# Performance work log

Hardware: AMD Instinct MI355X
Metric: run time of the kernel (lower is better)

Reference implementation:

```python
import jax, jax.numpy as jnp
import numpy as np

N, E, G, H, L, GD = 100000, 1600000, 64, 128, 3, 32
NEG_SLOPE = 0.2
EPS = 1e-5


def setup_inputs() -> dict:
    key = jax.random.key(0)
    ks = jax.random.split(key, 10)
    s = 1.0 / np.sqrt(H)
    return {
        "x": jax.random.normal(ks[0], (N, H), jnp.float32),
        "global_feat": jax.random.normal(ks[1], (G, GD), jnp.float32),
        "W_src": jax.random.normal(ks[2], (L, H, H), jnp.float32) * s,
        "W_dst": jax.random.normal(ks[3], (L, H, H), jnp.float32) * s,
        "att": jax.random.normal(ks[4], (L, H), jnp.float32) * s,
        "b_conv": jnp.zeros((L, H), jnp.float32),
        "gn_w": jnp.ones((L, H), jnp.float32),
        "gn_b": jnp.zeros((L, H), jnp.float32),
        "gn_ms": jnp.ones((L, H), jnp.float32),
        "W1": jax.random.normal(ks[5], (H * L + GD, H), jnp.float32) * (1.0 / np.sqrt(H * L + GD)),
        "b1": jnp.zeros((H,), jnp.float32),
        "W2": jax.random.normal(ks[6], (H, 1), jnp.float32) * s,
        "b2": jnp.zeros((1,), jnp.float32),
        "edge_index": jax.random.randint(ks[7], (2, E), 0, N, jnp.int64),
        "batch": jnp.sort(jax.random.randint(ks[8], (N,), 0, G, jnp.int64)),
    }


def reference(x, global_feat, W_src, W_dst, att, b_conv, gn_w, gn_b, gn_ms,
              W1, b1, W2, b2, edge_index, batch):
    n = x.shape[0]
    g = global_feat.shape[0]
    layers = W_src.shape[0]
    loops = jnp.arange(n, dtype=edge_index.dtype)
    src = jnp.concatenate([edge_index[0], loops])  # add_self_loops=True
    dst = jnp.concatenate([edge_index[1], loops])
    counts = jnp.maximum(
        jax.ops.segment_sum(jnp.ones((n,), x.dtype), batch, num_segments=g), 1.0)

    outs = []
    for l in range(layers):
        # --- GATv2Conv (heads=1) ---
        xl = x @ W_src[l]          # source transform [N,H]
        xr = x @ W_dst[l]          # target transform [N,H]
        e = jax.nn.leaky_relu(xl[src] + xr[dst], NEG_SLOPE) @ att[l]  # [Etot]
        emax = jax.ops.segment_max(e, dst, num_segments=n)
        ex = jnp.exp(e - emax[dst])
        denom = jax.ops.segment_sum(ex, dst, num_segments=n)
        alpha = ex / denom[dst]
        h = jax.ops.segment_sum(alpha[:, None] * xl[src], dst, num_segments=n) + b_conv[l]
        # --- GraphNorm ---
        mean = jax.ops.segment_sum(h, batch, num_segments=g) / counts[:, None]
        sub = h - gn_ms[l] * mean[batch]
        var = jax.ops.segment_sum(sub * sub, batch, num_segments=g) / counts[:, None]
        h = gn_w[l] * sub * jax.lax.rsqrt(var[batch] + EPS) + gn_b[l]
        x = jax.nn.relu(h)
        # --- global_mean_pool ---
        outs.append(jax.ops.segment_sum(x, batch, num_segments=g) / counts[:, None])

    hcat = jnp.concatenate(outs + [global_feat], axis=1)  # JK cat + global feats
    z = jax.nn.relu(hcat @ W1 + b1)  # dropout = identity (eval)
    return z @ W2 + b2
```

## Files before the change

### kernel.cpp

```cpp
#include <hip/hip_runtime.h>
#include <hip/hip_bf16.h>
#include <math.h>

#define N_    100000
#define E_    1600000
#define ETOT_ 1700000
#define G_    64
#define H_    128
#define GH_   8192
#define L_    3
#define GD_   32
#define NEG_  0.2f
#define EPS_  1e-5f

#define NBUK_ 391
#define CH_   2048
#define MCH_  782

typedef unsigned short ushort_t;
typedef unsigned int uint_t;
typedef __attribute__((ext_vector_type(4))) float f32x4;
typedef __attribute__((ext_vector_type(8))) short bf16x8;
typedef __attribute__((ext_vector_type(8))) unsigned short ushort8;

__device__ __forceinline__ ushort_t bfb(float f) {
    __hip_bfloat16 h = __float2bfloat16(f);
    return *reinterpret_cast<ushort_t*>(&h);
}
__device__ __forceinline__ float uf(ushort_t u) {
    return __uint_as_float(((uint_t)u) << 16);
}


__global__ void k_init(float* pooled, float* gsum, float* gsq, int* gstart,
                       const int* __restrict__ batch) {
    int i = blockIdx.x * 256 + threadIdx.x;
    if (i < L_ * GH_) { pooled[i] = 0.f; gsum[i] = 0.f; gsq[i] = 0.f; }
    if (i <= G_) {
        int lo = 0, hi = N_;
        while (lo < hi) { int mid = (lo + hi) >> 1; if (batch[mid] < i) lo = mid + 1; else hi = mid; }
        gstart[i] = lo;
    }
}


__global__ __launch_bounds__(256) void k_bcount(const int* __restrict__ edst, int* __restrict__ C) {
    __shared__ int hist[NBUK_];
    int t = threadIdx.x, m = blockIdx.x;
    for (int i = t; i < NBUK_; i += 256) hist[i] = 0;
    __syncthreads();
    int base = m * CH_;
#pragma unroll
    for (int j = 0; j < CH_ / 256; j++) {
        int e = base + j * 256 + t;
        if (e < E_) atomicAdd(&hist[edst[e] >> 8], 1);
    }
    __syncthreads();
    for (int i = t; i < NBUK_; i += 256) C[i * MCH_ + m] = hist[i];
}

__global__ __launch_bounds__(1024) void k_bscan(int* __restrict__ C, int* __restrict__ bucketEdges) {
    __shared__ int arr[1024];
    int b = blockIdx.x, t = threadIdx.x;
    int v = (t < MCH_) ? C[b * MCH_ + t] : 0;
    arr[t] = v;
    __syncthreads();
    for (int off = 1; off < 1024; off <<= 1) {
        int x = (t >= off) ? arr[t - off] : 0;
        __syncthreads();
        arr[t] += x;
        __syncthreads();
    }
    if (t < MCH_) C[b * MCH_ + t] = arr[t] - v;
    if (t == 1023) bucketEdges[b] = arr[1023];
}

__global__ __launch_bounds__(512) void k_bscan2(const int* __restrict__ bucketEdges,
                                                int* __restrict__ bstartE, int* __restrict__ bstartT,
                                                int* __restrict__ rowptr) {
    __shared__ int aE[512], aT[512];
    int t = threadIdx.x;
    int e = 0, tot = 0;
    if (t < NBUK_) {
        e = bucketEdges[t];
        int nib = N_ - t * 256; if (nib > 256) nib = 256;
        tot = e + nib;
    }
    aE[t] = e; aT[t] = tot;
    __syncthreads();
    for (int off = 1; off < 512; off <<= 1) {
        int xe = (t >= off) ? aE[t - off] : 0;
        int xt = (t >= off) ? aT[t - off] : 0;
        __syncthreads();
        aE[t] += xe; aT[t] += xt;
        __syncthreads();
    }
    if (t < NBUK_) { bstartE[t] = aE[t] - e; bstartT[t] = aT[t] - tot; }
    if (t == 0) rowptr[N_] = ETOT_;
}

__global__ __launch_bounds__(256) void k_bscatter(const int* __restrict__ esrc, const int* __restrict__ edst,
                                                  const int* __restrict__ C, const int* __restrict__ bstartE,
                                                  int2* __restrict__ stag) {
    __shared__ int cur[NBUK_];
    int t = threadIdx.x, m = blockIdx.x;
    for (int i = t; i < NBUK_; i += 256) cur[i] = C[i * MCH_ + m] + bstartE[i];
    __syncthreads();
    int base = m * CH_;
#pragma unroll
    for (int j = 0; j < CH_ / 256; j++) {
        int e = base + j * 256 + t;
        if (e < E_) {
            int s = esrc[e], d = edst[e];
            int pos = atomicAdd(&cur[d >> 8], 1);
            int2 p; p.x = s; p.y = d;
            stag[pos] = p;
        }
    }
}

__global__ __launch_bounds__(256) void k_bfinal(const int2* __restrict__ stag,
                                                const int* __restrict__ bucketEdges,
                                                const int* __restrict__ bstartE, const int* __restrict__ bstartT,
                                                int* __restrict__ rowptr, int* __restrict__ colarr) {
    __shared__ int deg[256];
    __shared__ int cursor[256];
    int b = blockIdx.x, t = threadIdx.x;
    int nb0 = b * 256;
    int nib = N_ - nb0; if (nib > 256) nib = 256;
    int ebeg = bstartE[b], ecnt = bucketEdges[b];
    deg[t] = (t < nib) ? 1 : 0;
    __syncthreads();
    for (int i = t; i < ecnt; i += 256) {
        int2 p = stag[ebeg + i];
        atomicAdd(&deg[p.y - nb0], 1);
    }
    __syncthreads();
    int v = deg[t];
    cursor[t] = v;
    __syncthreads();
    for (int off = 1; off < 256; off <<= 1) {
        int x = (t >= off) ? cursor[t - off] : 0;
        __syncthreads();
        cursor[t] += x;
        __syncthreads();
    }
    int excl = cursor[t] - v;
    int rowbase = bstartT[b];
    if (t < nib) {
        rowptr[nb0 + t] = rowbase + excl;
        colarr[rowbase + excl] = nb0 + t;
    }
    __syncthreads();
    cursor[t] = excl + 1;
    __syncthreads();
    for (int i = t; i < ecnt; i += 256) {
        int2 p = stag[ebeg + i];
        int pos = atomicAdd(&cursor[p.y - nb0], 1);
        colarr[rowbase + pos] = p.x;
    }
}


__global__ void k_prep_w(const float* __restrict__ Ws, const float* __restrict__ Wd,
                         ushort_t* __restrict__ Wt) {
    int i = blockIdx.x * 256 + threadIdx.x;
    if (i >= L_ * 256 * H_) return;
    int l = i >> 15;
    int r = i & 32767;
    int c = r >> 7, k = r & 127;
    float v = (c < H_) ? Ws[(size_t)l * H_ * H_ + k * H_ + c]
                       : Wd[(size_t)l * H_ * H_ + k * H_ + (c - H_)];
    Wt[i] = bfb(v);
}


template<int FIRST>
__global__ __launch_bounds__(256) void k_mfma_t(const float* __restrict__ x0,
                                                const ushort_t* __restrict__ hin,
                                                const int* __restrict__ batch,
                                                const float* __restrict__ mv,
                                                const float* __restrict__ iv,
                                                const float* __restrict__ bb,
                                                const ushort_t* __restrict__ Wt,
                                                ushort_t* __restrict__ xlb,
                                                ushort_t* __restrict__ xrb) {
    int wv = threadIdx.x >> 6, lane = threadIdx.x & 63;
    int row0 = (blockIdx.x * 4 + wv) * 16;
    if (row0 >= N_) return;
    int sl = lane & 15, q = lane >> 4;
    int row = row0 + sl;

    bf16x8 a[4];
    if (FIRST) {
        const float* ap = x0 + (size_t)row * H_ + q * 8;
#pragma unroll
        for (int kk = 0; kk < 4; kk++) {
            float4 v0 = *(const float4*)(ap + kk * 32);
            float4 v1 = *(const float4*)(ap + kk * 32 + 4);
            bf16x8 t;
            t[0] = (short)bfb(v0.x); t[1] = (short)bfb(v0.y);
            t[2] = (short)bfb(v0.z); t[3] = (short)bfb(v0.w);
            t[4] = (short)bfb(v1.x); t[5] = (short)bfb(v1.y);
            t[6] = (short)bfb(v1.z); t[7] = (short)bfb(v1.w);
            a[kk] = t;
        }
    } else {
        int g = batch[row];
        const ushort_t* hp = hin + (size_t)row * H_ + q * 8;
        const float* mvp = mv + g * H_ + q * 8;
        const float* ivp = iv + g * H_ + q * 8;
        const float* bbp = bb + q * 8;
#pragma unroll
        for (int kk = 0; kk < 4; kk++) {
            ushort8 u = *(const ushort8*)(hp + kk * 32);
            float4 m0 = *(const float4*)(mvp + kk * 32);
            float4 m1 = *(const float4*)(mvp + kk * 32 + 4);
            float4 i0 = *(const float4*)(ivp + kk * 32);
            float4 i1 = *(const float4*)(ivp + kk * 32 + 4);
            float4 c0 = *(const float4*)(bbp + kk * 32);
            float4 c1 = *(const float4*)(bbp + kk * 32 + 4);
            bf16x8 t;
            t[0] = (short)bfb(fmaxf((uf(u[0]) - m0.x) * i0.x + c0.x, 0.f));
            t[1] = (short)bfb(fmaxf((uf(u[1]) - m0.y) * i0.y + c0.y, 0.f));
            t[2] = (short)bfb(fmaxf((uf(u[2]) - m0.z) * i0.z + c0.z, 0.f));
            t[3] = (short)bfb(fmaxf((uf(u[3]) - m0.w) * i0.w + c0.w, 0.f));
            t[4] = (short)bfb(fmaxf((uf(u[4]) - m1.x) * i1.x + c1.x, 0.f));
            t[5] = (short)bfb(fmaxf((uf(u[5]) - m1.y) * i1.y + c1.y, 0.f));
            t[6] = (short)bfb(fmaxf((uf(u[6]) - m1.z) * i1.z + c1.z, 0.f));
            t[7] = (short)bfb(fmaxf((uf(u[7]) - m1.w) * i1.w + c1.w, 0.f));
            a[kk] = t;
        }
    }

    f32x4 acc[16];
#pragma unroll
    for (int c = 0; c < 16; c++) acc[c] = (f32x4){0.f, 0.f, 0.f, 0.f};

#pragma unroll
    for (int c = 0; c < 16; c++) {
        const ushort_t* bp = Wt + (size_t)(c * 16 + sl) * H_ + q * 8;
#pragma unroll
        for (int kk = 0; kk < 4; kk++) {
            bf16x8 b = *(const bf16x8*)(bp + kk * 32);
            acc[c] = __builtin_amdgcn_mfma_f32_16x16x32_bf16(a[kk], b, acc[c], 0, 0, 0);
        }
    }

    int orow = row0 + q * 4;
#pragma unroll
    for (int c = 0; c < 8; c++)
#pragma unroll
        for (int j = 0; j < 4; j++)
            xlb[(size_t)(orow + j) * H_ + c * 16 + sl] = bfb(acc[c][j]);
#pragma unroll
    for (int c = 8; c < 16; c++)
#pragma unroll
        for (int j = 0; j < 4; j++)
            xrb[(size_t)(orow + j) * H_ + (c - 8) * 16 + sl] = bfb(acc[c][j]);
}


__global__ __launch_bounds__(256) void k_conv(const ushort_t* __restrict__ xlb,
                                              const ushort_t* __restrict__ xrb,
                                              const int* __restrict__ rowptr, const int* __restrict__ colarr,
                                              const float* __restrict__ attl, const float* __restrict__ bcl,
                                              const int* __restrict__ batch,
                                              ushort_t* __restrict__ h,
                                              float* __restrict__ gsum, float* __restrict__ gsq) {
    __shared__ float ls1[H_], ls2[H_];
    int tid = threadIdx.x;
    if (tid < H_) { ls1[tid] = 0.f; ls2[tid] = 0.f; }
    __syncthreads();

    int lane = tid & 63, wv = tid >> 6;
    int sl = lane & 15, q = lane >> 4;
    int row = blockIdx.x * 16 + wv * 4 + q;
    int d0 = sl * 8;

    float xrv[8], av[8], av5[8];
    {
        ushort8 ux = *(const ushort8*)(xrb + (size_t)row * H_ + d0);
        float4 a0 = *(const float4*)(attl + d0);
        float4 a1 = *(const float4*)(attl + d0 + 4);
        av[0] = a0.x; av[1] = a0.y; av[2] = a0.z; av[3] = a0.w;
        av[4] = a1.x; av[5] = a1.y; av[6] = a1.z; av[7] = a1.w;
#pragma unroll
        for (int e = 0; e < 8; e++) { xrv[e] = uf(ux[e]); av5[e] = NEG_ * av[e]; }
    }

    int jb = rowptr[row];
    int n = rowptr[row + 1] - jb;

    float ssum = 0.f;
    float ac[8] = {0.f, 0.f, 0.f, 0.f, 0.f, 0.f, 0.f, 0.f};

    int s = (n > 0) ? colarr[jb] : 0;
    for (int i = 0; i < n; i++) {
        int snext = (i + 1 < n) ? colarr[jb + i + 1] : 0;
        ushort8 u = *(const ushort8*)(xlb + (size_t)s * H_ + d0);
        float v[8];
        float p = 0.f;
#pragma unroll
        for (int e = 0; e < 8; e++) {
            v[e] = uf(u[e]);
            float t = v[e] + xrv[e];
            p = fmaf(t, (t > 0.f ? av[e] : av5[e]), p);
        }
        p += __shfl_xor(p, 8);
        p += __shfl_xor(p, 4);
        p += __shfl_xor(p, 2);
        p += __shfl_xor(p, 1);
        float wgt = __expf(p);
        ssum += wgt;
#pragma unroll
        for (int e = 0; e < 8; e++) ac[e] = fmaf(wgt, v[e], ac[e]);
        s = snext;
    }

    float inv = 1.f / ssum;
    float4 b0 = *(const float4*)(bcl + d0);
    float4 b1 = *(const float4*)(bcl + d0 + 4);
    float o[8];
    o[0] = ac[0] * inv + b0.x; o[1] = ac[1] * inv + b0.y;
    o[2] = ac[2] * inv + b0.z; o[3] = ac[3] * inv + b0.w;
    o[4] = ac[4] * inv + b1.x; o[5] = ac[5] * inv + b1.y;
    o[6] = ac[6] * inv + b1.z; o[7] = ac[7] * inv + b1.w;

    ushort8 ho;
#pragma unroll
    for (int e = 0; e < 8; e++) ho[e] = bfb(o[e]);
    *(ushort8*)(h + (size_t)row * H_ + d0) = ho;

    float s1[8], s2[8];
#pragma unroll
    for (int e = 0; e < 8; e++) { s1[e] = o[e]; s2[e] = o[e] * o[e]; }

    int g0 = batch[blockIdx.x * 16];
    int g1 = batch[blockIdx.x * 16 + 15];
    if (g0 == g1) {
#pragma unroll
        for (int e = 0; e < 8; e++) {
            s1[e] += __shfl_xor(s1[e], 16); s1[e] += __shfl_xor(s1[e], 32);
            s2[e] += __shfl_xor(s2[e], 16); s2[e] += __shfl_xor(s2[e], 32);
        }
        if (q == 0) {
#pragma unroll
            for (int e = 0; e < 8; e++) {
                atomicAdd(&ls1[d0 + e], s1[e]);
                atomicAdd(&ls2[d0 + e], s2[e]);
            }
        }
        __syncthreads();
        if (tid < H_) atomicAdd(&gsum[g0 * H_ + tid], ls1[tid]);
        else if (tid < 2 * H_) atomicAdd(&gsq[g0 * H_ + tid - H_], ls2[tid - H_]);
    } else {
        int g = batch[row];
#pragma unroll
        for (int e = 0; e < 8; e++) {
            atomicAdd(&gsum[g * H_ + d0 + e], s1[e]);
            atomicAdd(&gsq[g * H_ + d0 + e], s2[e]);
        }
    }
}


__global__ void k_gn_fin(float* gsum, float* gsq, const int* __restrict__ gstart,
                         const float* __restrict__ gnwl, const float* __restrict__ gnmsl) {
    int i = blockIdx.x * 256 + threadIdx.x;
    if (i < GH_) {
        int g = i >> 7, d = i & 127;
        int c = gstart[g + 1] - gstart[g]; if (c < 1) c = 1;
        float ic = 1.f / (float)c;
        float mean = gsum[i] * ic;
        float e2   = gsq[i] * ic;
        float ms = gnmsl[d];
        float var = e2 - ms * (2.f - ms) * mean * mean;
        gsum[i] = ms * mean;
        gsq[i]  = gnwl[d] * rsqrtf(var + EPS_);
    }
}


__global__ void k_pool(const ushort_t* __restrict__ h, const int* __restrict__ batch,
                       const float* __restrict__ mv, const float* __restrict__ iv,
                       const float* __restrict__ bb, float* __restrict__ pooled_l) {
    int tid = threadIdx.x;
    int nb = blockIdx.x * 64;
    int d2 = (tid & 63) * 2, hh = tid >> 6;
    int nend = nb + 64; if (nend > N_) nend = N_;
    float b0 = bb[d2], b1 = bb[d2 + 1];
    float p0 = 0.f, p1 = 0.f; int curg = -1;
    float m0 = 0.f, m1 = 0.f, i0 = 0.f, i1 = 0.f;
    for (int n = nb + hh; n < nend; n += 4) {
        int g = batch[n];
        if (g != curg) {
            if (curg >= 0) {
                atomicAdd(&pooled_l[curg * H_ + d2], p0);
                atomicAdd(&pooled_l[curg * H_ + d2 + 1], p1);
            }
            p0 = 0.f; p1 = 0.f; curg = g;
            m0 = mv[g * H_ + d2]; m1 = mv[g * H_ + d2 + 1];
            i0 = iv[g * H_ + d2]; i1 = iv[g * H_ + d2 + 1];
        }
        uint_t u = *(const uint_t*)(h + (size_t)n * H_ + d2);
        float v0 = __uint_as_float(u << 16);
        float v1 = __uint_as_float(u & 0xffff0000u);
        v0 = fmaxf((v0 - m0) * i0 + b0, 0.f);
        v1 = fmaxf((v1 - m1) * i1 + b1, 0.f);
        p0 += v0; p1 += v1;
    }
    if (curg >= 0) {
        atomicAdd(&pooled_l[curg * H_ + d2], p0);
        atomicAdd(&pooled_l[curg * H_ + d2 + 1], p1);
    }
}


__global__ __launch_bounds__(128) void k_mlp(const float* __restrict__ pooled, const float* __restrict__ gfeat,
                                             const int* __restrict__ gstart,
                                             const float* __restrict__ W1, const float* __restrict__ b1,
                                             const float* __restrict__ W2, const float* __restrict__ b2,
                                             float* __restrict__ out) {
    int g = blockIdx.x;
    int c = threadIdx.x;
    __shared__ float hc[H_ * L_ + GD_];
    __shared__ float zz[H_];
    int cn = gstart[g + 1] - gstart[g]; if (cn < 1) cn = 1;
    float ic = 1.f / (float)cn;
    for (int k = c; k < H_ * L_; k += 128)
        hc[k] = pooled[(k >> 7) * GH_ + g * H_ + (k & 127)] * ic;
    if (c < GD_) hc[H_ * L_ + c] = gfeat[g * GD_ + c];
    __syncthreads();
    float z = b1[c];
#pragma unroll 4
    for (int k = 0; k < H_ * L_ + GD_; k++)
        z += hc[k] * W1[k * H_ + c];
    z = fmaxf(z, 0.f);
    zz[c] = z * W2[c];
    __syncthreads();
    for (int off = 64; off > 0; off >>= 1) {
        if (c < off) zz[c] += zz[c + off];
        __syncthreads();
    }
    if (c == 0) out[g] = zz[0] + b2[0];
}


extern "C" void kernel_launch(void* const* d_in, const int* in_sizes, int n_in,
                              void* d_out, int out_size, void* d_ws, size_t ws_size,
                              hipStream_t stream) {
    const float* x0    = (const float*)d_in[0];
    const float* gfeat = (const float*)d_in[1];
    const float* Wsrc  = (const float*)d_in[2];
    const float* Wdst  = (const float*)d_in[3];
    const float* att   = (const float*)d_in[4];
    const float* bconv = (const float*)d_in[5];
    const float* gnw   = (const float*)d_in[6];
    const float* gnb   = (const float*)d_in[7];
    const float* gnms  = (const float*)d_in[8];
    const float* W1    = (const float*)d_in[9];
    const float* b1    = (const float*)d_in[10];
    const float* W2    = (const float*)d_in[11];
    const float* b2    = (const float*)d_in[12];
    const int*   eidx  = (const int*)d_in[13];
    const int*   batch = (const int*)d_in[14];
    const int* esrc = eidx;
    const int* edst = eidx + E_;
    float* out = (float*)d_out;

    char* w = (char*)d_ws;
    size_t off = 0;
    auto alloc = [&](size_t bytes) { char* p = w + off; off += (bytes + 255) & ~(size_t)255; return p; };
    ushort_t* xlb  = (ushort_t*)alloc((size_t)N_ * H_ * 2);
    ushort_t* xrb  = (ushort_t*)alloc((size_t)N_ * H_ * 2);
    ushort_t* h    = (ushort_t*)alloc((size_t)N_ * H_ * 2);
    ushort_t* Wt   = (ushort_t*)alloc((size_t)L_ * 256 * H_ * 2);
    int*   rowptr  = (int*)alloc((size_t)(N_ + 1) * 4);
    int*   colarr  = (int*)alloc((size_t)ETOT_ * 4);
    int*   bktE    = (int*)alloc(NBUK_ * 4);
    int*   bstartE = (int*)alloc(NBUK_ * 4);
    int*   bstartT = (int*)alloc(NBUK_ * 4);
    int*   gstart  = (int*)alloc((G_ + 1) * 4);
    float* gsum    = (float*)alloc((size_t)L_ * GH_ * 4);
    float* gsq     = (float*)alloc((size_t)L_ * GH_ * 4);
    float* pooled  = (float*)alloc((size_t)L_ * GH_ * 4);
    int2* stag = (int2*)xlb;
    int*  C    = (int*)xrb;
    (void)ws_size; (void)in_sizes; (void)n_in; (void)out_size;

    k_init<<<(N_ + 255) / 256, 256, 0, stream>>>(pooled, gsum, gsq, gstart, batch);
    k_bcount<<<MCH_, 256, 0, stream>>>(edst, C);
    k_bscan<<<NBUK_, 1024, 0, stream>>>(C, bktE);
    k_bscan2<<<1, 512, 0, stream>>>(bktE, bstartE, bstartT, rowptr);
    k_bscatter<<<MCH_, 256, 0, stream>>>(esrc, edst, C, bstartE, stag);
    k_bfinal<<<NBUK_, 256, 0, stream>>>(stag, bktE, bstartE, bstartT, rowptr, colarr);
    k_prep_w<<<(L_ * 256 * H_ + 255) / 256, 256, 0, stream>>>(Wsrc, Wdst, Wt);

    int mfma_grid = (N_ / 16 + 3) / 4;
    for (int l = 0; l < L_; l++) {
        if (l == 0)
            k_mfma_t<1><<<mfma_grid, 256, 0, stream>>>(x0, h, batch, gsum, gsq, gnb,
                                                       Wt, xlb, xrb);
        else
            k_mfma_t<0><<<mfma_grid, 256, 0, stream>>>(x0, h, batch,
                                                       gsum + (size_t)(l - 1) * GH_,
                                                       gsq + (size_t)(l - 1) * GH_,
                                                       gnb + (size_t)(l - 1) * H_,
                                                       Wt + (size_t)l * 256 * H_, xlb, xrb);
        k_conv<<<N_ / 16, 256, 0, stream>>>(xlb, xrb, rowptr, colarr,
                                            att + (size_t)l * H_, bconv + (size_t)l * H_,
                                            batch, h,
                                            gsum + (size_t)l * GH_, gsq + (size_t)l * GH_);
        k_gn_fin<<<GH_ / 256, 256, 0, stream>>>(gsum + (size_t)l * GH_, gsq + (size_t)l * GH_,
                                                gstart, gnw + (size_t)l * H_, gnms + (size_t)l * H_);
        k_pool<<<(N_ + 63) / 64, 256, 0, stream>>>(h, batch,
                                                   gsum + (size_t)l * GH_, gsq + (size_t)l * GH_,
                                                   gnb + (size_t)l * H_, pooled + (size_t)l * GH_);
    }

    k_mlp<<<G_, 128, 0, stream>>>(pooled, gfeat, gstart, W1, b1, W2, b2, out);
}
```

Measured before the change: 741.1 us.

## Prefetch neighbor rows two ahead in GAT conv and split GraphNorm stats kernel

The edge-aggregation loop in k_conv now software-pipelines the gather, keeping two xl rows and one column index in flight ahead of use to hide memory latency on the irregular neighbor loads. The GraphNorm sum and sum-of-squares accumulation, with its shared-memory and global atomics, is moved out of k_conv into a new k_gn_stat kernel that re-reads h and accumulates per-graph partial sums. This lightens k_conv and its register and LDS use, but adds an extra launch and one more full pass over h per layer. Statistics are now computed from the bf16-rounded h instead of fp32 values.

```diff
diff --git a/kernel.cpp b/kernel.cpp
--- a/kernel.cpp
+++ b/kernel.cpp
@@ -265,14 +265,8 @@
                                               const ushort_t* __restrict__ xrb,
                                               const int* __restrict__ rowptr, const int* __restrict__ colarr,
                                               const float* __restrict__ attl, const float* __restrict__ bcl,
-                                              const int* __restrict__ batch,
-                                              ushort_t* __restrict__ h,
-                                              float* __restrict__ gsum, float* __restrict__ gsq) {
-    __shared__ float ls1[H_], ls2[H_];
+                                              ushort_t* __restrict__ h) {
     int tid = threadIdx.x;
-    if (tid < H_) { ls1[tid] = 0.f; ls2[tid] = 0.f; }
-    __syncthreads();
-
     int lane = tid & 63, wv = tid >> 6;
     int sl = lane & 15, q = lane >> 4;
     int row = blockIdx.x * 16 + wv * 4 + q;
@@ -291,19 +285,27 @@
 
     int jb = rowptr[row];
     int n = rowptr[row + 1] - jb;
+    int last = n - 1;
 
     float ssum = 0.f;
     float ac[8] = {0.f, 0.f, 0.f, 0.f, 0.f, 0.f, 0.f, 0.f};
 
-    int s = (n > 0) ? colarr[jb] : 0;
+    int c0 = colarr[jb];
+    int c1 = colarr[jb + (1 < last ? 1 : last)];
+    int sc = colarr[jb + (2 < last ? 2 : last)];
+    ushort8 u0 = *(const ushort8*)(xlb + (size_t)c0 * H_ + d0);
+    ushort8 u1 = *(const ushort8*)(xlb + (size_t)c1 * H_ + d0);
+
     for (int i = 0; i < n; i++) {
-        int snext = (i + 1 < n) ? colarr[jb + i + 1] : 0;
-        ushort8 u = *(const ushort8*)(xlb + (size_t)s * H_ + d0);
+        int i3 = i + 3; if (i3 > last) i3 = last;
+        int cn = colarr[jb + i3];
+        ushort8 u2 = *(const ushort8*)(xlb + (size_t)sc * H_ + d0);
+
         float v[8];
         float p = 0.f;
 #pragma unroll
         for (int e = 0; e < 8; e++) {
-            v[e] = uf(u[e]);
+            v[e] = uf(u0[e]);
             float t = v[e] + xrv[e];
             p = fmaf(t, (t > 0.f ? av[e] : av5[e]), p);
         }
@@ -315,52 +317,50 @@
         ssum += wgt;
 #pragma unroll
         for (int e = 0; e < 8; e++) ac[e] = fmaf(wgt, v[e], ac[e]);
-        s = snext;
+
+        u0 = u1; u1 = u2; sc = cn;
     }
 
     float inv = 1.f / ssum;
     float4 b0 = *(const float4*)(bcl + d0);
     float4 b1 = *(const float4*)(bcl + d0 + 4);
-    float o[8];
-    o[0] = ac[0] * inv + b0.x; o[1] = ac[1] * inv + b0.y;
-    o[2] = ac[2] * inv + b0.z; o[3] = ac[3] * inv + b0.w;
-    o[4] = ac[4] * inv + b1.x; o[5] = ac[5] * inv + b1.y;
-    o[6] = ac[6] * inv + b1.z; o[7] = ac[7] * inv + b1.w;
-
     ushort8 ho;
-#pragma unroll
-    for (int e = 0; e < 8; e++) ho[e] = bfb(o[e]);
+    ho[0] = bfb(ac[0] * inv + b0.x); ho[1] = bfb(ac[1] * inv + b0.y);
+    ho[2] = bfb(ac[2] * inv + b0.z); ho[3] = bfb(ac[3] * inv + b0.w);
+    ho[4] = bfb(ac[4] * inv + b1.x); ho[5] = bfb(ac[5] * inv + b1.y);
+    ho[6] = bfb(ac[6] * inv + b1.z); ho[7] = bfb(ac[7] * inv + b1.w);
     *(ushort8*)(h + (size_t)row * H_ + d0) = ho;
-
-    float s1[8], s2[8];
-#pragma unroll
-    for (int e = 0; e < 8; e++) { s1[e] = o[e]; s2[e] = o[e] * o[e]; }
-
-    int g0 = batch[blockIdx.x * 16];
-    int g1 = batch[blockIdx.x * 16 + 15];
-    if (g0 == g1) {
-#pragma unroll
-        for (int e = 0; e < 8; e++) {
-            s1[e] += __shfl_xor(s1[e], 16); s1[e] += __shfl_xor(s1[e], 32);
-            s2[e] += __shfl_xor(s2[e], 16); s2[e] += __shfl_xor(s2[e], 32);
-        }
-        if (q == 0) {
-#pragma unroll
-            for (int e = 0; e < 8; e++) {
-                atomicAdd(&ls1[d0 + e], s1[e]);
-                atomicAdd(&ls2[d0 + e], s2[e]);
+}
+
+
+__global__ void k_gn_stat(const ushort_t* __restrict__ h, const int* __restrict__ batch,
+                          float* gsum, float* gsq) {
+    int tid = threadIdx.x;
+    int nb = blockIdx.x * 64;
+    int d2 = (tid & 63) * 2, hh = tid >> 6;
+    int nend = nb + 64; if (nend > N_) nend = N_;
+    float s10 = 0.f, s11 = 0.f, s20 = 0.f, s21 = 0.f; int curg = -1;
+    for (int n = nb + hh; n < nend; n += 4) {
+        int g = batch[n];
+        if (g != curg) {
+            if (curg >= 0) {
+                atomicAdd(&gsum[curg * H_ + d2], s10);
+                atomicAdd(&gsum[curg * H_ + d2 + 1], s11);
+                atomicAdd(&gsq[curg * H_ + d2], s20);
+                atomicAdd(&gsq[curg * H_ + d2 + 1], s21);
             }
-        }
-        __syncthreads();
-        if (tid < H_) atomicAdd(&gsum[g0 * H_ + tid], ls1[tid]);
-        else if (tid < 2 * H_) atomicAdd(&gsq[g0 * H_ + tid - H_], ls2[tid - H_]);
-    } else {
-        int g = batch[row];
-#pragma unroll
-        for (int e = 0; e < 8; e++) {
-            atomicAdd(&gsum[g * H_ + d0 + e], s1[e]);
-            atomicAdd(&gsq[g * H_ + d0 + e], s2[e]);
-        }
+            s10 = s11 = s20 = s21 = 0.f; curg = g;
+        }
+        uint_t u = *(const uint_t*)(h + (size_t)n * H_ + d2);
+        float v0 = __uint_as_float(u << 16);
+        float v1 = __uint_as_float(u & 0xffff0000u);
+        s10 += v0; s11 += v1; s20 += v0 * v0; s21 += v1 * v1;
+    }
+    if (curg >= 0) {
+        atomicAdd(&gsum[curg * H_ + d2], s10);
+        atomicAdd(&gsum[curg * H_ + d2 + 1], s11);
+        atomicAdd(&gsq[curg * H_ + d2], s20);
+        atomicAdd(&gsq[curg * H_ + d2 + 1], s21);
     }
 }
 
@@ -509,9 +509,9 @@
                                                        gnb + (size_t)(l - 1) * H_,
                                                        Wt + (size_t)l * 256 * H_, xlb, xrb);
         k_conv<<<N_ / 16, 256, 0, stream>>>(xlb, xrb, rowptr, colarr,
-                                            att + (size_t)l * H_, bconv + (size_t)l * H_,
-                                            batch, h,
-                                            gsum + (size_t)l * GH_, gsq + (size_t)l * GH_);
+                                            att + (size_t)l * H_, bconv + (size_t)l * H_, h);
+        k_gn_stat<<<(N_ + 63) / 64, 256, 0, stream>>>(h, batch,
+                                                      gsum + (size_t)l * GH_, gsq + (size_t)l * GH_);
         k_gn_fin<<<GH_ / 256, 256, 0, stream>>>(gsum + (size_t)l * GH_, gsq + (size_t)l * GH_,
                                                 gstart, gnw + (size_t)l * H_, gnms + (size_t)l * H_);
         k_pool<<<(N_ + 63) / 64, 256, 0, stream>>>(h, batch,
```

After: 630.6 us. 1.18x faster.
